# Kernel optimization log

Measured on AMD Instinct MI355X. Metric: run time of the kernel, lower is better.

Reference implementation:

```python
import jax, jax.numpy as jnp
import numpy as np

DIM = 2048
N_HEADS = 16
HEAD_DIM = 128
KV_HEADS = 1
ROPE_BASE = 10000.0


def _rope_tables(T, dim, dtype):
    inv_freq = 1.0 / (ROPE_BASE ** (jnp.arange(0, dim, 2, dtype=jnp.float32) / dim))
    t = jnp.arange(T, dtype=jnp.float32)
    freqs = jnp.einsum('i,j->ij', t, inv_freq)          # [T, dim/2]
    emb = jnp.concatenate([freqs, freqs], axis=-1)      # [T, dim]
    cos = jnp.cos(emb)[None, None, :, :].astype(dtype)  # [1,1,T,dim]
    sin = jnp.sin(emb)[None, None, :, :].astype(dtype)
    return cos, sin


def _rotate_half(x):
    x1, x2 = jnp.split(x, 2, axis=-1)
    return jnp.concatenate([-x2, x1], axis=-1)


def setup_inputs() -> dict:
    key = jax.random.key(0)
    k1, k2, k3, k4, k5 = jax.random.split(key, 5)
    B, T = 2, 2048
    x = jax.random.normal(k1, (B, T, DIM), dtype=jnp.float32)
    # additive causal mask: 0 on/below diagonal, -1e9 above
    causal = jnp.triu(jnp.full((T, T), -1e9, dtype=jnp.float32), k=1)
    attn_mask = causal[None, None, :, :]
    s = 1.0 / np.sqrt(DIM)
    wq = jax.random.normal(k2, (DIM, N_HEADS * HEAD_DIM), dtype=jnp.float32) * s
    wk = jax.random.normal(k3, (DIM, KV_HEADS * HEAD_DIM), dtype=jnp.float32) * s
    wv = jax.random.normal(k4, (DIM, KV_HEADS * HEAD_DIM), dtype=jnp.float32) * s
    wo = jax.random.normal(k5, (N_HEADS * HEAD_DIM, DIM), dtype=jnp.float32) * s
    return {"x": x, "attn_mask": attn_mask, "wq": wq, "wk": wk, "wv": wv, "wo": wo}


def reference(x, attn_mask, wq, wk, wv, wo):
    B, T, C = x.shape
    q = (x @ wq).reshape(B, T, N_HEADS, HEAD_DIM).transpose(0, 2, 1, 3)   # [B,H,T,d]
    k = (x @ wk).reshape(B, T, KV_HEADS, HEAD_DIM).transpose(0, 2, 1, 3)  # [B,1,T,d]
    v = (x @ wv).reshape(B, T, KV_HEADS, HEAD_DIM).transpose(0, 2, 1, 3)  # [B,1,T,d]
    cos, sin = _rope_tables(T, HEAD_DIM, x.dtype)
    q = q * cos + _rotate_half(q) * sin
    k = k * cos + _rotate_half(k) * sin
    # KV head broadcasts over the H dim inside matmul (MQA expand path)
    att = jnp.matmul(q, k.swapaxes(-1, -2)) / np.sqrt(HEAD_DIM)          # [B,H,T,T]
    att = att + attn_mask
    w = jax.nn.softmax(att, axis=-1)
    y = jnp.matmul(w, v)                                                  # [B,H,T,d]
    y = y.transpose(0, 2, 1, 3).reshape(B, T, N_HEADS * HEAD_DIM)
    y = y @ wo
    k_exp = jnp.broadcast_to(k, (B, N_HEADS, T, HEAD_DIM))
    v_exp = jnp.broadcast_to(v, (B, N_HEADS, T, HEAD_DIM))
    return y, k_exp, v_exp
```

## Files before the change

### kernel.cpp

```cpp
#include <hip/hip_runtime.h>
#include <hip/hip_bf16.h>
#include <cstdint>
#include <cstddef>

#define B_SZ   2
#define T_SEQ  2048
#define C_DIM  2048
#define NH     16
#define HD     128

typedef __attribute__((ext_vector_type(8))) short s8v;
typedef __attribute__((ext_vector_type(4))) float f32x4;

typedef __attribute__((address_space(3))) char lds_char;
typedef __attribute__((address_space(1))) const char glob_char;

__device__ __forceinline__ unsigned short f2bf(float f) {
    union { float f; uint32_t i; } v; v.f = f;
    uint32_t r = (v.i + 0x7FFFu + ((v.i >> 16) & 1u)) >> 16;
    return (unsigned short)r;
}

__global__ void k_f32_to_bf16(const float* __restrict__ in,
                              unsigned short* __restrict__ out, int n4) {
    int i = blockIdx.x * blockDim.x + threadIdx.x;
    int stride = gridDim.x * blockDim.x;
    for (; i < n4; i += stride) {
        float4 v = reinterpret_cast<const float4*>(in)[i];
        ushort4 o;
        o.x = f2bf(v.x); o.y = f2bf(v.y); o.z = f2bf(v.z); o.w = f2bf(v.w);
        reinterpret_cast<ushort4*>(out)[i] = o;
    }
}

__global__ void k_transp_bf16(const float* __restrict__ in,
                              unsigned short* __restrict__ out,
                              int R, int C, int ldo) {
    __shared__ unsigned short tile[64][66];
    int x0 = blockIdx.x * 64, y0 = blockIdx.y * 64;
    int tx = threadIdx.x, ty = threadIdx.y;
#pragma unroll
    for (int j = 0; j < 16; ++j) {
        int r = y0 + ty + j * 4;
        tile[ty + j * 4][tx] = f2bf(in[(size_t)r * C + x0 + tx]);
    }
    __syncthreads();
#pragma unroll
    for (int j = 0; j < 16; ++j) {
        int orow = x0 + ty + j * 4;
        out[(size_t)orow * ldo + y0 + tx] = tile[tx][ty + j * 4];
    }
}

__global__ void k_rope_tab(float* __restrict__ cosT, float* __restrict__ sinT) {
    int idx = blockIdx.x * blockDim.x + threadIdx.x;
    if (idx >= T_SEQ * 64) return;
    int t = idx >> 6, i = idx & 63;
    float inv = powf(10000.0f, -(float)i / 64.0f);
    float ang = (float)t * inv;
    cosT[idx] = cosf(ang);
    sinT[idx] = sinf(ang);
}

#define BM 128
#define BN 128
#define BK 64

__global__ __launch_bounds__(256) void k_gemm_bt(
        const unsigned short* __restrict__ A,
        const unsigned short* __restrict__ Bt,
        float* __restrict__ C, int M, int N, int K, int ldc) {
    __shared__ char smem[BM * BK * 2 + BN * BK * 2];
    char* As = smem;
    char* Bs = smem + BM * BK * 2;
    int tid = threadIdx.x, lane = tid & 63, wid = tid >> 6;
    int m0 = blockIdx.y * BM, n0 = blockIdx.x * BN;
    int wr = wid >> 1, wc = wid & 1;

    f32x4 acc[4][4] = {};

    int srow = wid * 32 + (lane >> 3);
    int cp = lane & 7;

    for (int k0 = 0; k0 < K; k0 += BK) {
#pragma unroll
        for (int i = 0; i < 4; ++i) {
            int row = srow + i * 8;
            int c = cp ^ (row & 7);
            const unsigned short* ga = A + (size_t)(m0 + row) * K + k0 + c * 8;
            const unsigned short* gb = Bt + (size_t)(n0 + row) * K + k0 + c * 8;
            __builtin_amdgcn_global_load_lds((glob_char*)ga,
                (lds_char*)(As + wid * 4096 + i * 1024), 16, 0, 0);
            __builtin_amdgcn_global_load_lds((glob_char*)gb,
                (lds_char*)(Bs + wid * 4096 + i * 1024), 16, 0, 0);
        }
        __syncthreads();

#pragma unroll
        for (int kc = 0; kc < 2; ++kc) {
            s8v af[4], bfr[4];
#pragma unroll
            for (int mi = 0; mi < 4; ++mi) {
                int row = wr * 64 + mi * 16 + (lane & 15);
                int slot = (kc * 4 + (lane >> 4)) ^ (row & 7);
                af[mi] = *reinterpret_cast<const s8v*>(As + row * 128 + slot * 16);
            }
#pragma unroll
            for (int ni = 0; ni < 4; ++ni) {
                int row = wc * 64 + ni * 16 + (lane & 15);
                int slot = (kc * 4 + (lane >> 4)) ^ (row & 7);
                bfr[ni] = *reinterpret_cast<const s8v*>(Bs + row * 128 + slot * 16);
            }
#pragma unroll
            for (int mi = 0; mi < 4; ++mi)
#pragma unroll
                for (int ni = 0; ni < 4; ++ni)
                    acc[mi][ni] = __builtin_amdgcn_mfma_f32_16x16x32_bf16(
                        af[mi], bfr[ni], acc[mi][ni], 0, 0, 0);
        }
        __syncthreads();
    }

#pragma unroll
    for (int mi = 0; mi < 4; ++mi) {
        int row = m0 + wr * 64 + mi * 16 + ((lane >> 4) << 2);
#pragma unroll
        for (int ni = 0; ni < 4; ++ni) {
            int col = n0 + wc * 64 + ni * 16 + (lane & 15);
            float* cp2 = C + (size_t)row * ldc + col;
#pragma unroll
            for (int r = 0; r < 4; ++r)
                cp2[(size_t)r * ldc] = acc[mi][ni][r];
        }
    }
}

__global__ void k_qkv_transform(const float* __restrict__ qkv,
                                const float* __restrict__ cosT,
                                const float* __restrict__ sinT,
                                unsigned short* __restrict__ qB,
                                unsigned short* __restrict__ kB,
                                unsigned short* __restrict__ vT,
                                float* __restrict__ kexp,
                                float* __restrict__ vexp) {
    int bt = blockIdx.x;
    int b = bt >> 11, t = bt & 2047;
    int tid = threadIdx.x;
    const float* base = qkv + (size_t)bt * 2304;
    const float SCALE = 0.08838834764831845f;

    for (int i = tid; i < 1024; i += 256) {
        int h = i >> 6, d = i & 63;
        float c = cosT[t * 64 + d], s = sinT[t * 64 + d];
        float q1 = base[h * 128 + d], q2 = base[h * 128 + d + 64];
        float o1 = (q1 * c - q2 * s) * SCALE;
        float o2 = (q2 * c + q1 * s) * SCALE;
        size_t qoff = ((size_t)(b * NH + h) * T_SEQ + t) * HD + d;
        qB[qoff] = f2bf(o1);
        qB[qoff + 64] = f2bf(o2);
    }
    if (tid < 64) {
        int d = tid;
        float c = cosT[t * 64 + d], s = sinT[t * 64 + d];
        float k1 = base[2048 + d], k2 = base[2048 + d + 64];
        float o1 = k1 * c - k2 * s;
        float o2 = k2 * c + k1 * s;
        size_t koff = ((size_t)b * T_SEQ + t) * HD + d;
        kB[koff] = f2bf(o1);
        kB[koff + 64] = f2bf(o2);
#pragma unroll
        for (int h = 0; h < NH; ++h) {
            size_t eoff = ((size_t)(b * NH + h) * T_SEQ + t) * HD + d;
            kexp[eoff] = o1;
            kexp[eoff + 64] = o2;
        }
    }
    if (tid >= 128) {
        int d = tid - 128;
        float v = base[2176 + d];
        vT[((size_t)b * HD + d) * T_SEQ + t] = f2bf(v);
#pragma unroll
        for (int h = 0; h < NH; ++h)
            vexp[((size_t)(b * NH + h) * T_SEQ + t) * HD + d] = v;
    }
}

__global__ __launch_bounds__(256) void k_flash_attn(
        const unsigned short* __restrict__ qB,
        const unsigned short* __restrict__ kB,
        const unsigned short* __restrict__ vT,
        unsigned short* __restrict__ yattn) {
    __shared__ char smem[81920];
    int tid = threadIdx.x, lane = tid & 63, wvid = tid >> 6;
    int blk = blockIdx.x;
    int qt = 15 - (blk >> 5);
    int bh = blk & 31;
    int b = bh >> 4, h = bh & 15;
    int q0 = qt * 128 + wvid * 32;

    char* Ks0 = smem;
    char* Vs0 = smem + 32768;
    char* pbase = smem + 65536 + wvid * 4096;

    const unsigned short* kbB  = kB + (size_t)b * T_SEQ * HD;
    const unsigned short* vbase = vT + (size_t)b * HD * T_SEQ;

    const unsigned short* qbase = qB + ((size_t)(b * NH + h) * T_SEQ + q0) * HD;
    s8v aq[2][4];
#pragma unroll
    for (int rt = 0; rt < 2; ++rt)
#pragma unroll
        for (int kc = 0; kc < 4; ++kc) {
            int row = rt * 16 + (lane & 15);
            aq[rt][kc] = *reinterpret_cast<const s8v*>(
                qbase + (size_t)row * HD + kc * 32 + (lane >> 4) * 8);
        }

    float m_r[2][4], l_r[2][4];
#pragma unroll
    for (int rt = 0; rt < 2; ++rt)
#pragma unroll
        for (int r = 0; r < 4; ++r) { m_r[rt][r] = -3e38f; l_r[rt][r] = 0.f; }
    f32x4 o[2][8] = {};

    int NT = 2 * qt + 2;

    auto stage = [&](int buf, int t) {
        int kv0 = t * 64;
#pragma unroll
        for (int j = 0; j < 4; ++j) {
            int n = j * 256 + tid;
            int row = n >> 4, ch = n & 15;
            const unsigned short* src =
                kbB + (size_t)(kv0 + row) * HD + (ch ^ (row & 7)) * 8;
            __builtin_amdgcn_global_load_lds((glob_char*)src,
                (lds_char*)(Ks0 + buf * 16384 + j * 4096 + wvid * 1024), 16, 0, 0);
        }
#pragma unroll
        for (int j = 0; j < 4; ++j) {
            int n = j * 256 + tid;
            int row = n >> 3, ch = n & 7;
            const unsigned short* src =
                vbase + (size_t)row * T_SEQ + kv0 + (ch ^ (row & 7)) * 8;
            __builtin_amdgcn_global_load_lds((glob_char*)src,
                (lds_char*)(Vs0 + buf * 16384 + j * 4096 + wvid * 1024), 16, 0, 0);
        }
    };

    stage(0, 0);
    asm volatile("s_waitcnt vmcnt(0)" ::: "memory");
    __builtin_amdgcn_s_barrier();
    __builtin_amdgcn_sched_barrier(0);

    for (int t = 0; t < NT; ++t) {
        int cur = t & 1;
        if (t + 1 < NT) stage(cur ^ 1, t + 1);
        int kv0 = t * 64;
        const char* Kc = Ks0 + cur * 16384;
        const char* Vc = Vs0 + cur * 16384;

        f32x4 sfr[2][4] = {};
#pragma unroll
        for (int kc = 0; kc < 4; ++kc) {
            s8v kf[4];
#pragma unroll
            for (int n = 0; n < 4; ++n) {
                int row = n * 16 + (lane & 15);
                int byte = row * 256 +
                    ((kc * 64 + (lane >> 4) * 16) ^ ((row & 7) << 4));
                kf[n] = *reinterpret_cast<const s8v*>(Kc + byte);
            }
#pragma unroll
            for (int rt = 0; rt < 2; ++rt)
#pragma unroll
                for (int n = 0; n < 4; ++n)
                    sfr[rt][n] = __builtin_amdgcn_mfma_f32_16x16x32_bf16(
                        aq[rt][kc], kf[n], sfr[rt][n], 0, 0, 0);
        }

        if (kv0 + 63 > q0) {
#pragma unroll
            for (int rt = 0; rt < 2; ++rt)
#pragma unroll
                for (int n = 0; n < 4; ++n)
#pragma unroll
                    for (int r = 0; r < 4; ++r) {
                        int col = kv0 + n * 16 + (lane & 15);
                        int row = q0 + rt * 16 + ((lane >> 4) << 2) + r;
                        if (col > row) sfr[rt][n][r] = -1e9f;
                    }
        }

#pragma unroll
        for (int rt = 0; rt < 2; ++rt) {
            float alpha[4];
#pragma unroll
            for (int r = 0; r < 4; ++r) {
                float v0 = fmaxf(fmaxf(sfr[rt][0][r], sfr[rt][1][r]),
                                 fmaxf(sfr[rt][2][r], sfr[rt][3][r]));
#pragma unroll
                for (int off = 1; off < 16; off <<= 1)
                    v0 = fmaxf(v0, __shfl_xor(v0, off));
                float mn = fmaxf(m_r[rt][r], v0);
                alpha[r] = __expf(m_r[rt][r] - mn);
                m_r[rt][r] = mn;
            }
            float rs[4] = {0.f, 0.f, 0.f, 0.f};
#pragma unroll
            for (int n = 0; n < 4; ++n)
#pragma unroll
                for (int r = 0; r < 4; ++r) {
                    float p = __expf(sfr[rt][n][r] - m_r[rt][r]);
                    sfr[rt][n][r] = p;
                    rs[r] += p;
                }
#pragma unroll
            for (int r = 0; r < 4; ++r) {
                float v0 = rs[r];
#pragma unroll
                for (int off = 1; off < 16; off <<= 1)
                    v0 += __shfl_xor(v0, off);
                l_r[rt][r] = l_r[rt][r] * alpha[r] + v0;
#pragma unroll
                for (int ds = 0; ds < 8; ++ds)
                    o[rt][ds][r] *= alpha[r];
            }
        }

#pragma unroll
        for (int rt = 0; rt < 2; ++rt)
#pragma unroll
            for (int n = 0; n < 4; ++n)
#pragma unroll
                for (int r = 0; r < 4; ++r) {
                    int rowl = rt * 16 + ((lane >> 4) << 2) + r;
                    int byte = rowl * 128 + (n * 16 + (lane & 15)) * 2;
                    byte ^= ((rowl & 7) << 4);
                    *reinterpret_cast<unsigned short*>(pbase + byte) =
                        f2bf(sfr[rt][n][r]);
                }
        asm volatile("s_waitcnt lgkmcnt(0)" ::: "memory");
        __builtin_amdgcn_sched_barrier(0);

#pragma unroll
        for (int kc2 = 0; kc2 < 2; ++kc2) {
            s8v pa[2];
#pragma unroll
            for (int rt = 0; rt < 2; ++rt) {
                int rowl = rt * 16 + (lane & 15);
                int byte = rowl * 128 +
                    ((kc2 * 64 + (lane >> 4) * 16) ^ ((rowl & 7) << 4));
                pa[rt] = *reinterpret_cast<const s8v*>(pbase + byte);
            }
#pragma unroll
            for (int ds = 0; ds < 8; ++ds) {
                int vrow = ds * 16 + (lane & 15);
                int vbyte = vrow * 128 +
                    ((kc2 * 64 + (lane >> 4) * 16) ^ ((vrow & 7) << 4));
                s8v bv = *reinterpret_cast<const s8v*>(Vc + vbyte);
#pragma unroll
                for (int rt = 0; rt < 2; ++rt)
                    o[rt][ds] = __builtin_amdgcn_mfma_f32_16x16x32_bf16(
                        pa[rt], bv, o[rt][ds], 0, 0, 0);
            }
        }

        asm volatile("s_waitcnt vmcnt(0) lgkmcnt(0)" ::: "memory");
        __builtin_amdgcn_s_barrier();
        __builtin_amdgcn_sched_barrier(0);
    }

#pragma unroll
    for (int rt = 0; rt < 2; ++rt) {
        float inv[4];
#pragma unroll
        for (int r = 0; r < 4; ++r) inv[r] = 1.0f / l_r[rt][r];
#pragma unroll
        for (int ds = 0; ds < 8; ++ds)
#pragma unroll
            for (int r = 0; r < 4; ++r) {
                int row = q0 + rt * 16 + ((lane >> 4) << 2) + r;
                int col = h * HD + ds * 16 + (lane & 15);
                yattn[((size_t)b * T_SEQ + row) * C_DIM + col] =
                    f2bf(o[rt][ds][r] * inv[r]);
            }
    }
}

extern "C" void kernel_launch(void* const* d_in, const int* in_sizes, int n_in,
                              void* d_out, int out_size, void* d_ws, size_t ws_size,
                              hipStream_t stream) {
    const float* x  = (const float*)d_in[0];
    const float* wq = (const float*)d_in[2];
    const float* wk = (const float*)d_in[3];
    const float* wv = (const float*)d_in[4];
    const float* wo = (const float*)d_in[5];

    char* ws = (char*)d_ws;
    size_t off = 0;
    auto alloc = [&](size_t bytes) -> void* {
        void* p = ws + off;
        off += (bytes + 255) & ~(size_t)255;
        return p;
    };
    unsigned short* xb   = (unsigned short*)alloc((size_t)4096 * 2048 * 2);
    unsigned short* wT   = (unsigned short*)alloc((size_t)2304 * 2048 * 2);
    unsigned short* woT  = (unsigned short*)alloc((size_t)2048 * 2048 * 2);
    float*          qkv  = (float*)alloc((size_t)4096 * 2304 * 4);
    float*          cosT = (float*)alloc((size_t)2048 * 64 * 4);
    float*          sinT = (float*)alloc((size_t)2048 * 64 * 4);
    unsigned short* qB   = (unsigned short*)alloc((size_t)2 * 16 * 2048 * 128 * 2);
    unsigned short* kB   = (unsigned short*)alloc((size_t)2 * 2048 * 128 * 2);
    unsigned short* vT   = (unsigned short*)alloc((size_t)2 * 128 * 2048 * 2);
    unsigned short* yattn = (unsigned short*)qkv;

    float* y_out = (float*)d_out;
    float* kexp  = y_out + (size_t)2 * 2048 * 2048;
    float* vexp  = kexp + (size_t)2 * 16 * 2048 * 128;

    dim3 tb(64, 4);
    k_f32_to_bf16<<<2048, 256, 0, stream>>>(x, xb, 4096 * 2048 / 4);
    k_transp_bf16<<<dim3(32, 32), tb, 0, stream>>>(wq, wT, 2048, 2048, 2048);
    k_transp_bf16<<<dim3(2, 32), tb, 0, stream>>>(wk, wT + (size_t)2048 * 2048, 2048, 128, 2048);
    k_transp_bf16<<<dim3(2, 32), tb, 0, stream>>>(wv, wT + (size_t)2176 * 2048, 2048, 128, 2048);
    k_transp_bf16<<<dim3(32, 32), tb, 0, stream>>>(wo, woT, 2048, 2048, 2048);
    k_rope_tab<<<512, 256, 0, stream>>>(cosT, sinT);

    k_gemm_bt<<<dim3(2304 / BN, 4096 / BM), 256, 0, stream>>>(
        xb, wT, qkv, 4096, 2304, 2048, 2304);
    k_qkv_transform<<<4096, 256, 0, stream>>>(qkv, cosT, sinT, qB, kB, vT, kexp, vexp);
    k_flash_attn<<<512, 256, 0, stream>>>(qB, kB, vT, yattn);
    k_gemm_bt<<<dim3(2048 / BN, 4096 / BM), 256, 0, stream>>>(
        yattn, woT, y_out, 4096, 2048, 2048, 2048);
}
```

Baseline: 285.7 us.

## Use exp2 softmax with lazy rescaling, deferred row sums, setprio and hw bf16 cvt

Folds log2(e) into the Q scale so the softmax can use exp2 directly. Rescaling of the running max and accumulators is skipped unless some row's tile max exceeds the old max by more than 8, and the per-row sum stays as per-lane partials that are reduced by shuffles only once at the end. Also adds s_setprio around the MFMA blocks, uses the v_cvt_pk_bf16_f32 instruction for bf16 conversion, and sets a launch_bounds occupancy hint of 2. The intent is to remove per-tile shuffle reductions and exp/multiply work from the inner loop. The cost is that unnormalized probabilities can reach up to 2^8, which trades some bf16 precision headroom.

```diff
diff --git a/kernel.cpp b/kernel.cpp
--- a/kernel.cpp
+++ b/kernel.cpp
@@ -19,6 +19,12 @@
     union { float f; uint32_t i; } v; v.f = f;
     uint32_t r = (v.i + 0x7FFFu + ((v.i >> 16) & 1u)) >> 16;
     return (unsigned short)r;
+}
+
+__device__ __forceinline__ unsigned short cvt1_bf16(float f) {
+    unsigned int w;
+    asm("v_cvt_pk_bf16_f32 %0, %1, %2" : "=v"(w) : "v"(f), "v"(f));
+    return (unsigned short)w;
 }
 
 __global__ void k_f32_to_bf16(const float* __restrict__ in,
@@ -147,7 +153,7 @@
     int b = bt >> 11, t = bt & 2047;
     int tid = threadIdx.x;
     const float* base = qkv + (size_t)bt * 2304;
-    const float SCALE = 0.08838834764831845f;
+    const float SCALE = 0.08838834764831845f * 1.4426950408889634f;
 
     for (int i = tid; i < 1024; i += 256) {
         int h = i >> 6, d = i & 63;
@@ -185,7 +191,7 @@
     }
 }
 
-__global__ __launch_bounds__(256) void k_flash_attn(
+__global__ __launch_bounds__(256, 2) void k_flash_attn(
         const unsigned short* __restrict__ qB,
         const unsigned short* __restrict__ kB,
         const unsigned short* __restrict__ vT,
@@ -202,7 +208,7 @@
     char* Vs0 = smem + 32768;
     char* pbase = smem + 65536 + wvid * 4096;
 
-    const unsigned short* kbB  = kB + (size_t)b * T_SEQ * HD;
+    const unsigned short* kbB   = kB + (size_t)b * T_SEQ * HD;
     const unsigned short* vbase = vT + (size_t)b * HD * T_SEQ;
 
     const unsigned short* qbase = qB + ((size_t)(b * NH + h) * T_SEQ + q0) * HD;
@@ -260,6 +266,7 @@
         const char* Vc = Vs0 + cur * 16384;
 
         f32x4 sfr[2][4] = {};
+        __builtin_amdgcn_s_setprio(1);
 #pragma unroll
         for (int kc = 0; kc < 4; ++kc) {
             s8v kf[4];
@@ -277,6 +284,7 @@
                     sfr[rt][n] = __builtin_amdgcn_mfma_f32_16x16x32_bf16(
                         aq[rt][kc], kf[n], sfr[rt][n], 0, 0, 0);
         }
+        __builtin_amdgcn_s_setprio(0);
 
         if (kv0 + 63 > q0) {
 #pragma unroll
@@ -293,7 +301,7 @@
 
 #pragma unroll
         for (int rt = 0; rt < 2; ++rt) {
-            float alpha[4];
+            float pm[4];
 #pragma unroll
             for (int r = 0; r < 4; ++r) {
                 float v0 = fmaxf(fmaxf(sfr[rt][0][r], sfr[rt][1][r]),
@@ -301,30 +309,32 @@
 #pragma unroll
                 for (int off = 1; off < 16; off <<= 1)
                     v0 = fmaxf(v0, __shfl_xor(v0, off));
-                float mn = fmaxf(m_r[rt][r], v0);
-                alpha[r] = __expf(m_r[rt][r] - mn);
-                m_r[rt][r] = mn;
-            }
-            float rs[4] = {0.f, 0.f, 0.f, 0.f};
+                pm[r] = v0;
+            }
+            int ok = (pm[0] <= m_r[rt][0] + 8.0f) &
+                     (pm[1] <= m_r[rt][1] + 8.0f) &
+                     (pm[2] <= m_r[rt][2] + 8.0f) &
+                     (pm[3] <= m_r[rt][3] + 8.0f);
+            if (!__all(ok)) {
+#pragma unroll
+                for (int r = 0; r < 4; ++r) {
+                    float mn = fmaxf(m_r[rt][r], pm[r]);
+                    float al = exp2f(m_r[rt][r] - mn);
+                    l_r[rt][r] *= al;
+#pragma unroll
+                    for (int ds = 0; ds < 8; ++ds)
+                        o[rt][ds][r] *= al;
+                    m_r[rt][r] = mn;
+                }
+            }
 #pragma unroll
             for (int n = 0; n < 4; ++n)
 #pragma unroll
                 for (int r = 0; r < 4; ++r) {
-                    float p = __expf(sfr[rt][n][r] - m_r[rt][r]);
+                    float p = exp2f(sfr[rt][n][r] - m_r[rt][r]);
                     sfr[rt][n][r] = p;
-                    rs[r] += p;
+                    l_r[rt][r] += p;
                 }
-#pragma unroll
-            for (int r = 0; r < 4; ++r) {
-                float v0 = rs[r];
-#pragma unroll
-                for (int off = 1; off < 16; off <<= 1)
-                    v0 += __shfl_xor(v0, off);
-                l_r[rt][r] = l_r[rt][r] * alpha[r] + v0;
-#pragma unroll
-                for (int ds = 0; ds < 8; ++ds)
-                    o[rt][ds][r] *= alpha[r];
-            }
         }
 
 #pragma unroll
@@ -337,11 +347,12 @@
                     int byte = rowl * 128 + (n * 16 + (lane & 15)) * 2;
                     byte ^= ((rowl & 7) << 4);
                     *reinterpret_cast<unsigned short*>(pbase + byte) =
-                        f2bf(sfr[rt][n][r]);
+                        cvt1_bf16(sfr[rt][n][r]);
                 }
         asm volatile("s_waitcnt lgkmcnt(0)" ::: "memory");
         __builtin_amdgcn_sched_barrier(0);
 
+        __builtin_amdgcn_s_setprio(1);
 #pragma unroll
         for (int kc2 = 0; kc2 < 2; ++kc2) {
             s8v pa[2];
@@ -364,6 +375,7 @@
                         pa[rt], bv, o[rt][ds], 0, 0, 0);
             }
         }
+        __builtin_amdgcn_s_setprio(0);
 
         asm volatile("s_waitcnt vmcnt(0) lgkmcnt(0)" ::: "memory");
         __builtin_amdgcn_s_barrier();
@@ -374,7 +386,13 @@
     for (int rt = 0; rt < 2; ++rt) {
         float inv[4];
 #pragma unroll
-        for (int r = 0; r < 4; ++r) inv[r] = 1.0f / l_r[rt][r];
+        for (int r = 0; r < 4; ++r) {
+            float lv = l_r[rt][r];
+#pragma unroll
+            for (int off = 1; off < 16; off <<= 1)
+                lv += __shfl_xor(lv, off);
+            inv[r] = 1.0f / lv;
+        }
 #pragma unroll
         for (int ds = 0; ds < 8; ++ds)
 #pragma unroll
@@ -382,7 +400,7 @@
                 int row = q0 + rt * 16 + ((lane >> 4) << 2) + r;
                 int col = h * HD + ds * 16 + (lane & 15);
                 yattn[((size_t)b * T_SEQ + row) * C_DIM + col] =
-                    f2bf(o[rt][ds][r] * inv[r]);
+                    cvt1_bf16(o[rt][ds][r] * inv[r]);
             }
     }
 }
```

Result: faster. 269.8 us (-5.6%).
